# Optimization experiments

Hardware: AMD Instinct MI355X
Metric: run time of the kernel (lower is better)

The kernel has to match this reference:

```python
import jax, jax.numpy as jnp
import numpy as np

# Dims (match init_kwargs / input_specs)
W_STEPS, E, B, I, F = 128, 16, 64, 8, 64
P = 8 + F  # proj_size = 72


def setup_inputs() -> dict:
    key = jax.random.key(0)
    ks = jax.random.split(key, 8)
    N = B * I
    inputs = jax.random.normal(ks[0], (W_STEPS, E, B, I, F), dtype=jnp.float32)
    state = jnp.zeros((1, E, N, 1), dtype=jnp.float32)
    # linear projection params (xavier-uniform-ish scale)
    lim_lin = np.sqrt(6.0 / (P + F))
    weight_linear = jax.random.uniform(ks[1], (E, P, F), jnp.float32, -lim_lin, lim_lin)
    bias_linear = jnp.zeros((E, P), dtype=jnp.float32)
    # per-ensemble GRU params, hidden_size=1: gate order (r, z, n) as in torch
    lim = 1.0  # torch GRU init: U(-1/sqrt(hidden)=1, 1)
    w_ih = jax.random.uniform(ks[2], (E, 3, P), jnp.float32, -lim, lim)
    w_hh = jax.random.uniform(ks[3], (E, 3), jnp.float32, -lim, lim)
    b_ih = jax.random.uniform(ks[4], (E, 3), jnp.float32, -lim, lim)
    b_hh = jax.random.uniform(ks[5], (E, 3), jnp.float32, -lim, lim)
    return {"inputs": inputs, "state": state, "weight_linear": weight_linear,
            "bias_linear": bias_linear, "w_ih": w_ih, "w_hh": w_hh,
            "b_ih": b_ih, "b_hh": b_hh}


def reference(inputs, state, weight_linear, bias_linear, w_ih, w_hh, b_ih, b_hh):
    W, E_, B_, I_, F_ = inputs.shape
    N = B_ * I_
    x = inputs.reshape(W, E_, N, F_)
    h0 = state[-1].reshape(E_, N)  # hidden_size = 1 -> squeeze last dim
    # y[w,e,n,p] = sum_f weight_linear[e,p,f] * x[w,e,n,f] + bias
    y = jnp.einsum('epf,wenf->wenp', weight_linear, x) + bias_linear[:, None, :]
    # precompute input-side gate activations for all timesteps: (W, E, N, 3)
    gx = jnp.einsum('egp,wenp->weng', w_ih, y) + b_ih[:, None, :]

    def step(h, gxt):
        # hidden-side gates: h (E,N) * w_hh (E,3) -> (E,N,3)
        gh = h[:, :, None] * w_hh[:, None, :] + b_hh[:, None, :]
        r = jax.nn.sigmoid(gxt[..., 0] + gh[..., 0])
        z = jax.nn.sigmoid(gxt[..., 1] + gh[..., 1])
        n = jnp.tanh(gxt[..., 2] + r * gh[..., 2])
        h_new = (1.0 - z) * n + z * h
        return h_new, h_new

    _, outs = jax.lax.scan(step, h0, gx)  # outs: (W, E, N)
    return outs.reshape(W, E_, B_, I_, 1)
```

## Files before the change

### kernel.cpp

```cpp
#include <hip/hip_runtime.h>

#define WD 128
#define ED 16
#define ND 512
#define FD 64
#define PD 72

__global__ __launch_bounds__(256) void gru_prep(
    const float* __restrict__ wl,
    const float* __restrict__ bl,
    const float* __restrict__ wih,
    const float* __restrict__ bih,
    float* __restrict__ ws)
{
    const int t = threadIdx.x;
    float* Wc = ws;
    float* bc = ws + ED * 3 * FD;

    #pragma unroll
    for (int k = 0; k < 12; ++k) {
        const int idx = t + 256 * k;
        const int f  = idx & 63;
        const int eg = idx >> 6;
        const int e  = idx / 192;
        const float* a = wih + eg * PD;
        const float* w = wl + (size_t)e * PD * FD + f;
        float s = 0.0f;
        for (int p = 0; p < PD; ++p) s = fmaf(a[p], w[p * FD], s);
        Wc[idx] = s;
    }
    if (t < ED * 3) {
        const int e = t / 3;
        const float* a = wih + t * PD;
        const float* b = bl + (size_t)e * PD;
        float s = bih[t];
        for (int p = 0; p < PD; ++p) s = fmaf(a[p], b[p], s);
        bc[t] = s;
    }
}

__global__ __launch_bounds__(256) void gru_main(
    const float* __restrict__ x,
    const float* __restrict__ st,
    const float* __restrict__ whh,
    const float* __restrict__ bhh,
    const float* __restrict__ ws,
    float* __restrict__ out)
{
    const int lane = threadIdx.x & 63;
    const int gw   = (blockIdx.x << 2) + (threadIdx.x >> 6);
    const int e    = gw >> 6;
    const int n    = ((gw & 63) << 3) + (lane >> 3);
    const int c    = lane & 7;

    const float* Wc = ws;
    const float* bc = ws + ED * 3 * FD;

    const float4 wA0 = *(const float4*)(Wc + (e * 3 + 0) * FD + c * 8);
    const float4 wB0 = *(const float4*)(Wc + (e * 3 + 0) * FD + c * 8 + 4);
    const float4 wA1 = *(const float4*)(Wc + (e * 3 + 1) * FD + c * 8);
    const float4 wB1 = *(const float4*)(Wc + (e * 3 + 1) * FD + c * 8 + 4);
    const float4 wA2 = *(const float4*)(Wc + (e * 3 + 2) * FD + c * 8);
    const float4 wB2 = *(const float4*)(Wc + (e * 3 + 2) * FD + c * 8 + 4);
    const float bc0 = bc[e * 3 + 0], bc1 = bc[e * 3 + 1], bc2 = bc[e * 3 + 2];
    const float wh0 = whh[e * 3 + 0], wh1 = whh[e * 3 + 1], wh2 = whh[e * 3 + 2];
    const float bh0 = bhh[e * 3 + 0], bh1 = bhh[e * 3 + 1], bh2 = bhh[e * 3 + 2];

    float h = st[e * ND + n];

    const float* px = x + ((size_t)e * ND + n) * FD + c * 8;
    const size_t xstr = (size_t)ED * ND * FD;
    float* po = out + (size_t)e * ND + n;
    const size_t ostr = (size_t)ED * ND;

    float4 a0, b0, a1, b1, a2, b2, a3, b3;
    a0 = *(const float4*)px; b0 = *(const float4*)(px + 4); px += xstr;
    a1 = *(const float4*)px; b1 = *(const float4*)(px + 4); px += xstr;
    a2 = *(const float4*)px; b2 = *(const float4*)(px + 4); px += xstr;
    a3 = *(const float4*)px; b3 = *(const float4*)(px + 4); px += xstr;

#define GRU_STEP(AA, BB)                                                        \
    {                                                                           \
        float s0, s1, s2;                                                       \
        s0 = AA.x * wA0.x;            s1 = AA.x * wA1.x;            s2 = AA.x * wA2.x; \
        s0 = fmaf(AA.y, wA0.y, s0);   s1 = fmaf(AA.y, wA1.y, s1);   s2 = fmaf(AA.y, wA2.y, s2); \
        s0 = fmaf(AA.z, wA0.z, s0);   s1 = fmaf(AA.z, wA1.z, s1);   s2 = fmaf(AA.z, wA2.z, s2); \
        s0 = fmaf(AA.w, wA0.w, s0);   s1 = fmaf(AA.w, wA1.w, s1);   s2 = fmaf(AA.w, wA2.w, s2); \
        s0 = fmaf(BB.x, wB0.x, s0);   s1 = fmaf(BB.x, wB1.x, s1);   s2 = fmaf(BB.x, wB2.x, s2); \
        s0 = fmaf(BB.y, wB0.y, s0);   s1 = fmaf(BB.y, wB1.y, s1);   s2 = fmaf(BB.y, wB2.y, s2); \
        s0 = fmaf(BB.z, wB0.z, s0);   s1 = fmaf(BB.z, wB1.z, s1);   s2 = fmaf(BB.z, wB2.z, s2); \
        s0 = fmaf(BB.w, wB0.w, s0);   s1 = fmaf(BB.w, wB1.w, s1);   s2 = fmaf(BB.w, wB2.w, s2); \
        s0 += __shfl_xor(s0, 1, 64);  s1 += __shfl_xor(s1, 1, 64);  s2 += __shfl_xor(s2, 1, 64); \
        s0 += __shfl_xor(s0, 2, 64);  s1 += __shfl_xor(s1, 2, 64);  s2 += __shfl_xor(s2, 2, 64); \
        s0 += __shfl_xor(s0, 4, 64);  s1 += __shfl_xor(s1, 4, 64);  s2 += __shfl_xor(s2, 4, 64); \
        const float gh0 = fmaf(h, wh0, bh0);                                    \
        const float gh1 = fmaf(h, wh1, bh1);                                    \
        const float gh2 = fmaf(h, wh2, bh2);                                    \
        const float rr = 1.0f / (1.0f + expf(-(s0 + bc0 + gh0)));               \
        const float zz = 1.0f / (1.0f + expf(-(s1 + bc1 + gh1)));               \
        const float nn = tanhf(fmaf(rr, gh2, s2 + bc2));                        \
        h = fmaf(zz, h - nn, nn);                                               \
        if (c == 0) *po = h;                                                    \
        po += ostr;                                                             \
    }

    for (int w4 = 0; w4 < WD; w4 += 4) {
        const bool pf = (w4 + 4) < WD;
        {
            const float4 A = a0, B = b0;
            if (pf) { a0 = *(const float4*)px; b0 = *(const float4*)(px + 4); px += xstr; }
            GRU_STEP(A, B);
        }
        {
            const float4 A = a1, B = b1;
            if (pf) { a1 = *(const float4*)px; b1 = *(const float4*)(px + 4); px += xstr; }
            GRU_STEP(A, B);
        }
        {
            const float4 A = a2, B = b2;
            if (pf) { a2 = *(const float4*)px; b2 = *(const float4*)(px + 4); px += xstr; }
            GRU_STEP(A, B);
        }
        {
            const float4 A = a3, B = b3;
            if (pf) { a3 = *(const float4*)px; b3 = *(const float4*)(px + 4); px += xstr; }
            GRU_STEP(A, B);
        }
    }
#undef GRU_STEP
}

extern "C" void kernel_launch(void* const* d_in, const int* in_sizes, int n_in,
                              void* d_out, int out_size, void* d_ws, size_t ws_size,
                              hipStream_t stream)
{
    const float* x    = (const float*)d_in[0];
    const float* st   = (const float*)d_in[1];
    const float* wl   = (const float*)d_in[2];
    const float* bl   = (const float*)d_in[3];
    const float* wih  = (const float*)d_in[4];
    const float* whh  = (const float*)d_in[5];
    const float* bih  = (const float*)d_in[6];
    const float* bhh  = (const float*)d_in[7];
    float* out = (float*)d_out;
    float* ws  = (float*)d_ws;

    hipLaunchKernelGGL(gru_prep, dim3(1), dim3(256), 0, stream,
                       wl, bl, wih, bih, ws);
    hipLaunchKernelGGL(gru_main, dim3(256), dim3(256), 0, stream,
                       x, st, whh, bhh, ws, out);
}
```

Before: 404.5 us.

## Widen GRU parallel split, deepen prefetch, fast activations, parallel prep

The weight-folding prep kernel now runs as 48 blocks of 64 threads, with the bias dot product done by a wavefront shuffle reduction instead of a single block. The main kernel splits each row across 16 lanes of 4 features rather than 8 lanes of 8, doubling the grid to 512 blocks for more parallelism in the latency-bound recurrence. Prefetch depth goes from 4 to 8 timesteps. Sigmoid and tanh are replaced by exp2/rcp hardware intrinsics with pre-folded biases. This trades an extra shuffle stage and slightly lower activation accuracy for shorter per-step latency and more waves in flight.

```diff
diff --git a/kernel.cpp b/kernel.cpp
--- a/kernel.cpp
+++ b/kernel.cpp
@@ -6,37 +6,43 @@
 #define FD 64
 #define PD 72
 
-__global__ __launch_bounds__(256) void gru_prep(
+#define LOG2E  1.44269504088896340736f
+#define LOG2E2 2.88539008177792681472f
+__device__ __forceinline__ float fast_sig(float x) {
+    return __builtin_amdgcn_rcpf(1.0f + __builtin_amdgcn_exp2f(-LOG2E * x));
+}
+__device__ __forceinline__ float fast_tanh(float x) {
+    return 1.0f - 2.0f * __builtin_amdgcn_rcpf(1.0f + __builtin_amdgcn_exp2f(LOG2E2 * x));
+}
+
+__global__ __launch_bounds__(64) void gru_prep(
     const float* __restrict__ wl,
     const float* __restrict__ bl,
     const float* __restrict__ wih,
     const float* __restrict__ bih,
     float* __restrict__ ws)
 {
-    const int t = threadIdx.x;
-    float* Wc = ws;
-    float* bc = ws + ED * 3 * FD;
+    const int eg = blockIdx.x;
+    const int e  = eg / 3;
+    const int f  = threadIdx.x;
 
-    #pragma unroll
-    for (int k = 0; k < 12; ++k) {
-        const int idx = t + 256 * k;
-        const int f  = idx & 63;
-        const int eg = idx >> 6;
-        const int e  = idx / 192;
-        const float* a = wih + eg * PD;
-        const float* w = wl + (size_t)e * PD * FD + f;
-        float s = 0.0f;
-        for (int p = 0; p < PD; ++p) s = fmaf(a[p], w[p * FD], s);
-        Wc[idx] = s;
-    }
-    if (t < ED * 3) {
-        const int e = t / 3;
-        const float* a = wih + t * PD;
-        const float* b = bl + (size_t)e * PD;
-        float s = bih[t];
-        for (int p = 0; p < PD; ++p) s = fmaf(a[p], b[p], s);
-        bc[t] = s;
-    }
+    const float* a = wih + eg * PD;
+    const float* w = wl + (size_t)e * PD * FD + f;
+    float s = 0.0f;
+    #pragma unroll 8
+    for (int p = 0; p < PD; ++p) s = fmaf(a[p], w[p * FD], s);
+    ws[eg * FD + f] = s;
+
+    const float* b = bl + (size_t)e * PD;
+    float pv = a[f] * b[f];
+    if (f < 8) pv = fmaf(a[64 + f], b[64 + f], pv);
+    pv += __shfl_xor(pv, 1, 64);
+    pv += __shfl_xor(pv, 2, 64);
+    pv += __shfl_xor(pv, 4, 64);
+    pv += __shfl_xor(pv, 8, 64);
+    pv += __shfl_xor(pv, 16, 64);
+    pv += __shfl_xor(pv, 32, 64);
+    if (f == 0) ws[ED * 3 * FD + eg] = pv + bih[eg];
 }
 
 __global__ __launch_bounds__(256) void gru_main(
@@ -49,83 +55,68 @@
 {
     const int lane = threadIdx.x & 63;
     const int gw   = (blockIdx.x << 2) + (threadIdx.x >> 6);
-    const int e    = gw >> 6;
-    const int n    = ((gw & 63) << 3) + (lane >> 3);
-    const int c    = lane & 7;
+    const int e    = gw >> 7;
+    const int r    = lane >> 4;
+    const int n    = ((gw & 127) << 2) + r;
+    const int c    = lane & 15;
 
     const float* Wc = ws;
     const float* bc = ws + ED * 3 * FD;
 
-    const float4 wA0 = *(const float4*)(Wc + (e * 3 + 0) * FD + c * 8);
-    const float4 wB0 = *(const float4*)(Wc + (e * 3 + 0) * FD + c * 8 + 4);
-    const float4 wA1 = *(const float4*)(Wc + (e * 3 + 1) * FD + c * 8);
-    const float4 wB1 = *(const float4*)(Wc + (e * 3 + 1) * FD + c * 8 + 4);
-    const float4 wA2 = *(const float4*)(Wc + (e * 3 + 2) * FD + c * 8);
-    const float4 wB2 = *(const float4*)(Wc + (e * 3 + 2) * FD + c * 8 + 4);
-    const float bc0 = bc[e * 3 + 0], bc1 = bc[e * 3 + 1], bc2 = bc[e * 3 + 2];
+    const float4 w0 = *(const float4*)(Wc + (e * 3 + 0) * FD + c * 4);
+    const float4 w1 = *(const float4*)(Wc + (e * 3 + 1) * FD + c * 4);
+    const float4 w2 = *(const float4*)(Wc + (e * 3 + 2) * FD + c * 4);
     const float wh0 = whh[e * 3 + 0], wh1 = whh[e * 3 + 1], wh2 = whh[e * 3 + 2];
-    const float bh0 = bhh[e * 3 + 0], bh1 = bhh[e * 3 + 1], bh2 = bhh[e * 3 + 2];
+    const float B0 = bc[e * 3 + 0] + bhh[e * 3 + 0];
+    const float B1 = bc[e * 3 + 1] + bhh[e * 3 + 1];
+    const float bc2 = bc[e * 3 + 2];
+    const float bh2 = bhh[e * 3 + 2];
 
     float h = st[e * ND + n];
 
-    const float* px = x + ((size_t)e * ND + n) * FD + c * 8;
+    const float* px = x + ((size_t)e * ND + n) * FD + c * 4;
     const size_t xstr = (size_t)ED * ND * FD;
     float* po = out + (size_t)e * ND + n;
     const size_t ostr = (size_t)ED * ND;
 
-    float4 a0, b0, a1, b1, a2, b2, a3, b3;
-    a0 = *(const float4*)px; b0 = *(const float4*)(px + 4); px += xstr;
-    a1 = *(const float4*)px; b1 = *(const float4*)(px + 4); px += xstr;
-    a2 = *(const float4*)px; b2 = *(const float4*)(px + 4); px += xstr;
-    a3 = *(const float4*)px; b3 = *(const float4*)(px + 4); px += xstr;
+    float4 q0, q1, q2, q3, q4, q5, q6, q7;
+    q0 = *(const float4*)px; px += xstr;
+    q1 = *(const float4*)px; px += xstr;
+    q2 = *(const float4*)px; px += xstr;
+    q3 = *(const float4*)px; px += xstr;
+    q4 = *(const float4*)px; px += xstr;
+    q5 = *(const float4*)px; px += xstr;
+    q6 = *(const float4*)px; px += xstr;
+    q7 = *(const float4*)px; px += xstr;
 
-#define GRU_STEP(AA, BB)                                                        \
+#define GRU_STEP(XV)                                                            \
     {                                                                           \
-        float s0, s1, s2;                                                       \
-        s0 = AA.x * wA0.x;            s1 = AA.x * wA1.x;            s2 = AA.x * wA2.x; \
-        s0 = fmaf(AA.y, wA0.y, s0);   s1 = fmaf(AA.y, wA1.y, s1);   s2 = fmaf(AA.y, wA2.y, s2); \
-        s0 = fmaf(AA.z, wA0.z, s0);   s1 = fmaf(AA.z, wA1.z, s1);   s2 = fmaf(AA.z, wA2.z, s2); \
-        s0 = fmaf(AA.w, wA0.w, s0);   s1 = fmaf(AA.w, wA1.w, s1);   s2 = fmaf(AA.w, wA2.w, s2); \
-        s0 = fmaf(BB.x, wB0.x, s0);   s1 = fmaf(BB.x, wB1.x, s1);   s2 = fmaf(BB.x, wB2.x, s2); \
-        s0 = fmaf(BB.y, wB0.y, s0);   s1 = fmaf(BB.y, wB1.y, s1);   s2 = fmaf(BB.y, wB2.y, s2); \
-        s0 = fmaf(BB.z, wB0.z, s0);   s1 = fmaf(BB.z, wB1.z, s1);   s2 = fmaf(BB.z, wB2.z, s2); \
-        s0 = fmaf(BB.w, wB0.w, s0);   s1 = fmaf(BB.w, wB1.w, s1);   s2 = fmaf(BB.w, wB2.w, s2); \
-        s0 += __shfl_xor(s0, 1, 64);  s1 += __shfl_xor(s1, 1, 64);  s2 += __shfl_xor(s2, 1, 64); \
-        s0 += __shfl_xor(s0, 2, 64);  s1 += __shfl_xor(s1, 2, 64);  s2 += __shfl_xor(s2, 2, 64); \
-        s0 += __shfl_xor(s0, 4, 64);  s1 += __shfl_xor(s1, 4, 64);  s2 += __shfl_xor(s2, 4, 64); \
-        const float gh0 = fmaf(h, wh0, bh0);                                    \
-        const float gh1 = fmaf(h, wh1, bh1);                                    \
-        const float gh2 = fmaf(h, wh2, bh2);                                    \
-        const float rr = 1.0f / (1.0f + expf(-(s0 + bc0 + gh0)));               \
-        const float zz = 1.0f / (1.0f + expf(-(s1 + bc1 + gh1)));               \
-        const float nn = tanhf(fmaf(rr, gh2, s2 + bc2));                        \
+        float s0 = XV.x * w0.x, s1 = XV.x * w1.x, s2 = XV.x * w2.x;             \
+        s0 = fmaf(XV.y, w0.y, s0); s1 = fmaf(XV.y, w1.y, s1); s2 = fmaf(XV.y, w2.y, s2); \
+        s0 = fmaf(XV.z, w0.z, s0); s1 = fmaf(XV.z, w1.z, s1); s2 = fmaf(XV.z, w2.z, s2); \
+        s0 = fmaf(XV.w, w0.w, s0); s1 = fmaf(XV.w, w1.w, s1); s2 = fmaf(XV.w, w2.w, s2); \
+        s0 += __shfl_xor(s0, 1, 64); s1 += __shfl_xor(s1, 1, 64); s2 += __shfl_xor(s2, 1, 64); \
+        s0 += __shfl_xor(s0, 2, 64); s1 += __shfl_xor(s1, 2, 64); s2 += __shfl_xor(s2, 2, 64); \
+        s0 += __shfl_xor(s0, 4, 64); s1 += __shfl_xor(s1, 4, 64); s2 += __shfl_xor(s2, 4, 64); \
+        s0 += __shfl_xor(s0, 8, 64); s1 += __shfl_xor(s1, 8, 64); s2 += __shfl_xor(s2, 8, 64); \
+        const float rr = fast_sig(s0 + fmaf(h, wh0, B0));                       \
+        const float zz = fast_sig(s1 + fmaf(h, wh1, B1));                       \
+        const float nn = fast_tanh(fmaf(rr, fmaf(h, wh2, bh2), s2 + bc2));      \
         h = fmaf(zz, h - nn, nn);                                               \
         if (c == 0) *po = h;                                                    \
         po += ostr;                                                             \
     }
 
-    for (int w4 = 0; w4 < WD; w4 += 4) {
-        const bool pf = (w4 + 4) < WD;
-        {
-            const float4 A = a0, B = b0;
-            if (pf) { a0 = *(const float4*)px; b0 = *(const float4*)(px + 4); px += xstr; }
-            GRU_STEP(A, B);
-        }
-        {
-            const float4 A = a1, B = b1;
-            if (pf) { a1 = *(const float4*)px; b1 = *(const float4*)(px + 4); px += xstr; }
-            GRU_STEP(A, B);
-        }
-        {
-            const float4 A = a2, B = b2;
-            if (pf) { a2 = *(const float4*)px; b2 = *(const float4*)(px + 4); px += xstr; }
-            GRU_STEP(A, B);
-        }
-        {
-            const float4 A = a3, B = b3;
-            if (pf) { a3 = *(const float4*)px; b3 = *(const float4*)(px + 4); px += xstr; }
-            GRU_STEP(A, B);
-        }
+    for (int it = 0; it < WD / 8; ++it) {
+        const bool pf = it < (WD / 8 - 1);
+        { const float4 X = q0; if (pf) { q0 = *(const float4*)px; px += xstr; } GRU_STEP(X); }
+        { const float4 X = q1; if (pf) { q1 = *(const float4*)px; px += xstr; } GRU_STEP(X); }
+        { const float4 X = q2; if (pf) { q2 = *(const float4*)px; px += xstr; } GRU_STEP(X); }
+        { const float4 X = q3; if (pf) { q3 = *(const float4*)px; px += xstr; } GRU_STEP(X); }
+        { const float4 X = q4; if (pf) { q4 = *(const float4*)px; px += xstr; } GRU_STEP(X); }
+        { const float4 X = q5; if (pf) { q5 = *(const float4*)px; px += xstr; } GRU_STEP(X); }
+        { const float4 X = q6; if (pf) { q6 = *(const float4*)px; px += xstr; } GRU_STEP(X); }
+        { const float4 X = q7; if (pf) { q7 = *(const float4*)px; px += xstr; } GRU_STEP(X); }
     }
 #undef GRU_STEP
 }
@@ -145,8 +136,8 @@
     float* out = (float*)d_out;
     float* ws  = (float*)d_ws;
 
-    hipLaunchKernelGGL(gru_prep, dim3(1), dim3(256), 0, stream,
+    hipLaunchKernelGGL(gru_prep, dim3(48), dim3(64), 0, stream,
                        wl, bl, wih, bih, ws);
-    hipLaunchKernelGGL(gru_main, dim3(256), dim3(256), 0, stream,
+    hipLaunchKernelGGL(gru_main, dim3(512), dim3(256), 0, stream,
                        x, st, whh, bhh, ws, out);
 }
```

Result: faster. 375.4 us (median of 2 runs) (-7.2%).
